# Performance work log

Hardware: AMD Instinct MI355X
Metric: run time of the kernel (lower is better)

The kernel has to match this reference:

```python
import jax, jax.numpy as jnp
import numpy as np

NMS_RADIUS = 2.0   # cfgs.NMS_radius (meters)
EPS = 1e-6         # torch nn.PairwiseDistance default eps (added to the diff)
M = 16384          # number of keypoint candidates
SCENE = 100.0      # scene extent in meters


def setup_inputs() -> dict:
    key = jax.random.key(0)
    k1, k2 = jax.random.split(key)
    nodes = jax.random.uniform(k1, (M, 3), dtype=jnp.float32) * SCENE
    overlap_score = jax.random.normal(k2, (M,), dtype=jnp.float32)
    return {"nodes": nodes, "overlap_score": overlap_score}


def _greedy_nms(nodes, radius):
    """Sequential greedy NMS: keep node i iff its distance to every
    already-kept node exceeds radius. Faithful to the torch loop:
    (dis > radius).sum() == n_kept  <=>  all kept dists > radius."""
    n = nodes.shape[0]

    def body(i, mask):
        # torch nn.PairwiseDistance computes ||x1 - x2 + eps||_2
        d = jnp.linalg.norm(nodes[i] - nodes + EPS, axis=-1)  # [n]
        keep = jnp.all(jnp.where(mask, d > radius, True))
        return mask.at[i].set(keep)

    mask0 = jnp.zeros(n, dtype=bool).at[0].set(True)
    return jax.lax.fori_loop(1, n, body, mask0)


def reference(nodes, overlap_score):
    # sort by overlap score descending, run greedy NMS, unsort the mask
    order = jnp.argsort(-overlap_score)
    mask_sorted = _greedy_nms(nodes[order], NMS_RADIUS)
    mask = jnp.zeros_like(mask_sorted).at[order].set(mask_sorted)
    nms_length = mask.sum(dtype=jnp.int32)[None]
    return mask, nms_length
```

## Files before the change

### kernel.cpp

```cpp
#include <hip/hip_runtime.h>


#define M_PTS    16384
#define RADIUS   2.0f
#define EPS_D    1e-6f
#define GRID_N   25
#define NCELLS   (GRID_N * GRID_N * GRID_N)
#define CELL_CAP 12
#define K_NBR    12
#define CELLS_PB (GRID_N * GRID_N)
#define LIST_PB  (CELLS_PB * CELL_CAP)
#define EPT      5
#define ACT_PAD  (EPT * 1024)
#define SENT     M_PTS


__device__ __forceinline__ int cell_of(float v) {
  int c = (int)(v * 0.25f);
  return c < 0 ? 0 : (c > GRID_N - 1 ? GRID_N - 1 : c);
}

__device__ __forceinline__ bool edge_test(float4 pi, float4 pj, int j, int i) {
  bool earlier = (pj.w > pi.w) || ((pj.w == pi.w) && (j < i));
  if (!earlier) return false;
  float ddx = __fadd_rn(__fsub_rn(pi.x, pj.x), EPS_D);
  float ddy = __fadd_rn(__fsub_rn(pi.y, pj.y), EPS_D);
  float ddz = __fadd_rn(__fsub_rn(pi.z, pj.z), EPS_D);
  float d2 = __fadd_rn(__fadd_rn(__fmul_rn(ddx, ddx), __fmul_rn(ddy, ddy)),
                       __fmul_rn(ddz, ddz));
  return !(__fsqrt_rn(d2) > RADIUS);
}

__global__ __launch_bounds__(1024) void bin25(
    const float* __restrict__ nodes, const float* __restrict__ score,
    float4* __restrict__ pts, int* __restrict__ cell_cnt,
    unsigned short* __restrict__ cell_list) {
  __shared__ int ccnt[CELLS_PB];
  __shared__ unsigned short clist[LIST_PB];
  const int tid = threadIdx.x;
  const int b   = blockIdx.x;
  if (tid < CELLS_PB) ccnt[tid] = 0;
  __syncthreads();

  for (int i = tid; i < M_PTS; i += 1024) {
    float x = nodes[3 * i + 0];
    if (cell_of(x) != b) continue;
    float y = nodes[3 * i + 1];
    float z = nodes[3 * i + 2];
    float s = score[i];
    pts[i] = make_float4(x, y, z, s);
    int lc = cell_of(y) * GRID_N + cell_of(z);
    int pos = atomicAdd(&ccnt[lc], 1);
    if (pos < CELL_CAP) clist[lc * CELL_CAP + pos] = (unsigned short)i;
  }
  __syncthreads();

  if (tid < CELLS_PB) {
    int v = ccnt[tid];
    cell_cnt[b * CELLS_PB + tid] = v > CELL_CAP ? CELL_CAP : v;
  }
  for (int e = tid; e < LIST_PB; e += 1024)
    cell_list[b * LIST_PB + e] = clist[e];
}

__global__ __launch_bounds__(256) void wscan(
    const float4* __restrict__ pts, const int* __restrict__ cell_cnt,
    const unsigned short* __restrict__ cell_list,
    int* __restrict__ cnt, unsigned short* __restrict__ nbr,
    int* __restrict__ out) {
  const int tid  = threadIdx.x;
  const int lane = tid & 63;
  const int d    = lane & 31;
  const int half = lane >> 5;
  const int gwave = (blockIdx.x * 256 + tid) >> 6;
  const int i = gwave * 2 + half;

  const float4 pi = pts[i];
  int n = 0, cid = 0, m = 0, firstj = 0;
  if (d < 27) {
    int cx = cell_of(pi.x) + d / 9 - 1;
    int cy = cell_of(pi.y) + (d / 3) % 3 - 1;
    int cz = cell_of(pi.z) + d % 3 - 1;
    if (cx >= 0 && cx < GRID_N && cy >= 0 && cy < GRID_N &&
        cz >= 0 && cz < GRID_N) {
      cid = (cx * GRID_N + cy) * GRID_N + cz;
      m = cell_cnt[cid];
      for (int s = 0; s < m; ++s) {
        int j = cell_list[cid * CELL_CAP + s];
        if (edge_test(pi, pts[j], j, i)) { if (!n) firstj = j; ++n; }
      }
    }
  }
  int x = n;
#pragma unroll
  for (int off = 1; off < 32; off <<= 1) {
    int y = __shfl_up(x, off, 32);
    if (d >= off) x += y;
  }
  int excl = x - n;
  int tot = __shfl(x, 31, 32);
  if (n == 1) {
    if (excl < K_NBR) nbr[i * K_NBR + excl] = (unsigned short)firstj;
  } else if (n > 1) {
    int pos = excl;
    for (int s = 0; s < m && pos < K_NBR; ++s) {
      int j = cell_list[cid * CELL_CAP + s];
      if (edge_test(pi, pts[j], j, i)) {
        nbr[i * K_NBR + pos] = (unsigned short)j;
        ++pos;
      }
    }
  }
  if (d == 0) {
    cnt[i] = tot > K_NBR ? K_NBR : tot;
    if (tot == 0) out[i] = 1;
  }
}

__global__ __launch_bounds__(1024) void solve_nb(
    const int* __restrict__ cnt, const unsigned short* __restrict__ nbr,
    int* __restrict__ out, int out_size) {
  __shared__ unsigned char mask[M_PTS + 4];
  __shared__ unsigned int act[ACT_PAD];
  __shared__ int act_n, total;

  const int tid = threadIdx.x;
  const int lane = tid & 63;
  if (tid == 0) { act_n = 0; total = 0; }
  unsigned int* mask4 = (unsigned int*)mask;
  for (int w = tid; w < M_PTS / 4; w += 1024) mask4[w] = 0x01010101u;
  if (tid == 0) mask4[M_PTS / 4] = 0u;
  for (int a = tid; a < ACT_PAD; a += 1024) act[a] = 0u;
  __syncthreads();

  for (int k = tid; k < M_PTS; k += 1024) {
    int c = cnt[k];
    if (c > K_NBR) c = K_NBR;
    unsigned long long b = __ballot(c > 0);
    int wcnt = __popcll(b);
    int wbase = 0;
    if (lane == 0 && wcnt) wbase = atomicAdd(&act_n, wcnt);
    wbase = __shfl(wbase, 0, 64);
    if (c > 0) {
      int pos = wbase + __popcll(b & ((1ull << lane) - 1ull));
      if (pos < ACT_PAD) act[pos] = (unsigned)k | ((unsigned)c << 16);
    }
  }
  __syncthreads();
  const int na = act_n;
  const bool ok = (na <= ACT_PAD);

  unsigned ae[EPT];
  unsigned short r0[EPT], r1[EPT], r2[EPT];
  int cur[EPT];
#pragma unroll
  for (int e = 0; e < EPT; ++e) {
    unsigned v = act[tid + e * 1024];
    ae[e] = v;
    int k = (int)(v & 0xFFFFu);
    int c = (int)(v >> 16);
    const unsigned short* row = nbr + (size_t)k * K_NBR;
    unsigned w = (c > 0) ? *(const unsigned int*)row : 0u;
    r0[e] = (c > 0) ? (unsigned short)(w & 0xFFFFu) : (unsigned short)SENT;
    r1[e] = (c > 1) ? (unsigned short)(w >> 16)     : (unsigned short)SENT;
    r2[e] = (c > 2) ? row[2]                        : (unsigned short)SENT;
    cur[e] = 1;
  }
  __syncthreads();

  if (ok) {
    for (int it = 0; it < 96; ++it) {
      int m0[EPT], m1[EPT], m2[EPT];
#pragma unroll
      for (int e = 0; e < EPT; ++e) m0[e] = (int)mask[r0[e]];
#pragma unroll
      for (int e = 0; e < EPT; ++e) m1[e] = (int)mask[r1[e]];
#pragma unroll
      for (int e = 0; e < EPT; ++e) m2[e] = (int)mask[r2[e]];
      int any = 0;
#pragma unroll
      for (int e = 0; e < EPT; ++e) {
        unsigned v = ae[e];
        int c = (int)(v >> 16);
        if (!c) continue;
        int kp = (m0[e] ^ 1) & (m1[e] ^ 1) & (m2[e] ^ 1);
        if (c > 3) {
          int k = (int)(v & 0xFFFFu);
          const unsigned short* row = nbr + (size_t)k * K_NBR;
          for (int t = 3; t < c; ++t) kp &= (int)mask[row[t]] ^ 1;
        }
        if (kp != cur[e]) {
          cur[e] = kp;
          mask[v & 0xFFFFu] = (unsigned char)kp;
          any = 1;
        }
      }
      if (__syncthreads_count(any) == 0) break;
    }
    int ks = 0;
#pragma unroll
    for (int e = 0; e < EPT; ++e) {
      unsigned v = ae[e];
      if ((v >> 16) != 0u) {
        out[v & 0xFFFFu] = cur[e];
        ks += cur[e];
      }
    }
#pragma unroll
    for (int off = 32; off > 0; off >>= 1) ks += __shfl_down(ks, off, 64);
    if (lane == 0) atomicAdd(&total, ks);
    __syncthreads();
    if (tid == 0) out[out_size - 1] = (M_PTS - na) + total;
  } else {
    __shared__ int changed;
    for (int it = 0; it < 512; ++it) {
      if (tid == 0) changed = 0;
      __syncthreads();
      int any = 0;
      for (int k = tid; k < M_PTS; k += 1024) {
        int c = cnt[k]; if (c > K_NBR) c = K_NBR;
        if (!c) continue;
        int kp = 1;
        for (int t = 0; t < c; ++t) kp &= (int)mask[nbr[k * K_NBR + t]] ^ 1;
        if (kp != (int)mask[k]) { mask[k] = (unsigned char)kp; any = 1; }
      }
      if (any) changed = 1;
      __syncthreads();
      if (!changed) break;
    }
    __syncthreads();
    int ks = 0;
    for (int k = tid; k < M_PTS; k += 1024) {
      int m = (int)mask[k];
      out[k] = m;
      ks += m;
    }
#pragma unroll
    for (int off = 32; off > 0; off >>= 1) ks += __shfl_down(ks, off, 64);
    if (lane == 0) atomicAdd(&total, ks);
    __syncthreads();
    if (tid == 0) out[out_size - 1] = total;
  }
}

extern "C" void kernel_launch(void* const* d_in, const int* in_sizes, int n_in,
                              void* d_out, int out_size, void* d_ws, size_t ws_size,
                              hipStream_t stream) {
  const float* nodes = (const float*)d_in[0];
  const float* score = (const float*)d_in[1];
  int* out = (int*)d_out;

  char* ws = (char*)d_ws;
  float4* pts = (float4*)ws;
  int* cell_cnt = (int*)(ws + 262144);
  int* cnt = (int*)(ws + 327680);
  unsigned short* cell_list = (unsigned short*)(ws + 393216);
  unsigned short* nbr = (unsigned short*)(ws + 770048);

  bin25<<<GRID_N, 1024, 0, stream>>>(nodes, score, pts, cell_cnt, cell_list);
  wscan<<<2048, 256, 0, stream>>>(pts, cell_cnt, cell_list, cnt, nbr, out);
  solve_nb<<<1, 1024, 0, stream>>>(cnt, nbr, out, out_size);
}
```

Baseline: 39.43 us.

## Split active NMS nodes by degree and double-pump relaxation per barrier

The single-block fixed-point solver now sorts active nodes into two compact lists: nodes with exactly one earlier neighbour, stored as 16-bit ids with a cached neighbour, and nodes with two or more neighbours. Each iteration runs two relaxation sweeps between block-wide barriers, with a lower iteration cap. This aims to cut the number of __syncthreads_count barriers and to make the common single-neighbour case cheaper in registers and shared-memory reads. The cost is more work per barrier, and there is a risk of overflow into the slow fallback if either list exceeds its capacity.

```diff
diff --git a/kernel.cpp b/kernel.cpp
--- a/kernel.cpp
+++ b/kernel.cpp
@@ -10,9 +10,12 @@
 #define K_NBR    12
 #define CELLS_PB (GRID_N * GRID_N)
 #define LIST_PB  (CELLS_PB * CELL_CAP)
-#define EPT      5
-#define ACT_PAD  (EPT * 1024)
+#define EPT1     4
+#define C1_PAD   (EPT1 * 1024)
+#define EPT2     2
+#define C2_PAD   (EPT2 * 1024)
 #define SENT     M_PTS
+#define NOK1     0xFFFFu
 
 
 __device__ __forceinline__ int cell_of(float v) {
@@ -117,45 +120,69 @@
   }
 }
 
-__global__ __launch_bounds__(1024) void solve_nb(
+__global__ __launch_bounds__(1024) void solve_sp(
     const int* __restrict__ cnt, const unsigned short* __restrict__ nbr,
     int* __restrict__ out, int out_size) {
   __shared__ unsigned char mask[M_PTS + 4];
-  __shared__ unsigned int act[ACT_PAD];
-  __shared__ int act_n, total;
+  __shared__ unsigned short act1[C1_PAD];
+  __shared__ unsigned int  act2[C2_PAD];
+  __shared__ int n1_, n2_, total;
 
   const int tid = threadIdx.x;
   const int lane = tid & 63;
-  if (tid == 0) { act_n = 0; total = 0; }
+  if (tid == 0) { n1_ = 0; n2_ = 0; total = 0; }
   unsigned int* mask4 = (unsigned int*)mask;
   for (int w = tid; w < M_PTS / 4; w += 1024) mask4[w] = 0x01010101u;
   if (tid == 0) mask4[M_PTS / 4] = 0u;
-  for (int a = tid; a < ACT_PAD; a += 1024) act[a] = 0u;
+  unsigned int* act1w = (unsigned int*)act1;
+  for (int a = tid; a < C1_PAD / 2; a += 1024) act1w[a] = 0xFFFFFFFFu;
+  for (int a = tid; a < C2_PAD; a += 1024) act2[a] = 0u;
   __syncthreads();
 
   for (int k = tid; k < M_PTS; k += 1024) {
     int c = cnt[k];
     if (c > K_NBR) c = K_NBR;
-    unsigned long long b = __ballot(c > 0);
-    int wcnt = __popcll(b);
-    int wbase = 0;
-    if (lane == 0 && wcnt) wbase = atomicAdd(&act_n, wcnt);
-    wbase = __shfl(wbase, 0, 64);
-    if (c > 0) {
-      int pos = wbase + __popcll(b & ((1ull << lane) - 1ull));
-      if (pos < ACT_PAD) act[pos] = (unsigned)k | ((unsigned)c << 16);
-    }
-  }
-  __syncthreads();
-  const int na = act_n;
-  const bool ok = (na <= ACT_PAD);
-
-  unsigned ae[EPT];
-  unsigned short r0[EPT], r1[EPT], r2[EPT];
-  int cur[EPT];
-#pragma unroll
-  for (int e = 0; e < EPT; ++e) {
-    unsigned v = act[tid + e * 1024];
+    bool s1 = (c == 1), s2 = (c >= 2);
+    unsigned long long b1 = __ballot(s1);
+    if (b1) {
+      int wbase = 0;
+      if (lane == 0) wbase = atomicAdd(&n1_, __popcll(b1));
+      wbase = __shfl(wbase, 0, 64);
+      if (s1) {
+        int pos = wbase + __popcll(b1 & ((1ull << lane) - 1ull));
+        if (pos < C1_PAD) act1[pos] = (unsigned short)k;
+      }
+    }
+    unsigned long long b2 = __ballot(s2);
+    if (b2) {
+      int wbase = 0;
+      if (lane == 0) wbase = atomicAdd(&n2_, __popcll(b2));
+      wbase = __shfl(wbase, 0, 64);
+      if (s2) {
+        int pos = wbase + __popcll(b2 & ((1ull << lane) - 1ull));
+        if (pos < C2_PAD) act2[pos] = (unsigned)k | ((unsigned)c << 16);
+      }
+    }
+  }
+  __syncthreads();
+  const int n1 = n1_, n2 = n2_;
+  const bool ok = (n1 <= C1_PAD) && (n2 <= C2_PAD);
+
+  unsigned short k1[EPT1], q0[EPT1];
+  int cur1[EPT1];
+#pragma unroll
+  for (int e = 0; e < EPT1; ++e) {
+    unsigned short k = act1[tid + e * 1024];
+    k1[e] = k;
+    q0[e] = (k != NOK1) ? nbr[(size_t)k * K_NBR] : (unsigned short)SENT;
+    cur1[e] = 1;
+  }
+  unsigned ae[EPT2];
+  unsigned short r0[EPT2], r1[EPT2], r2[EPT2];
+  int cur2[EPT2];
+#pragma unroll
+  for (int e = 0; e < EPT2; ++e) {
+    unsigned v = act2[tid + e * 1024];
     ae[e] = v;
     int k = (int)(v & 0xFFFFu);
     int c = (int)(v >> 16);
@@ -164,53 +191,75 @@
     r0[e] = (c > 0) ? (unsigned short)(w & 0xFFFFu) : (unsigned short)SENT;
     r1[e] = (c > 1) ? (unsigned short)(w >> 16)     : (unsigned short)SENT;
     r2[e] = (c > 2) ? row[2]                        : (unsigned short)SENT;
-    cur[e] = 1;
+    cur2[e] = 1;
   }
   __syncthreads();
 
   if (ok) {
-    for (int it = 0; it < 96; ++it) {
-      int m0[EPT], m1[EPT], m2[EPT];
-#pragma unroll
-      for (int e = 0; e < EPT; ++e) m0[e] = (int)mask[r0[e]];
-#pragma unroll
-      for (int e = 0; e < EPT; ++e) m1[e] = (int)mask[r1[e]];
-#pragma unroll
-      for (int e = 0; e < EPT; ++e) m2[e] = (int)mask[r2[e]];
+    for (int it = 0; it < 48; ++it) {
       int any = 0;
 #pragma unroll
-      for (int e = 0; e < EPT; ++e) {
-        unsigned v = ae[e];
-        int c = (int)(v >> 16);
-        if (!c) continue;
-        int kp = (m0[e] ^ 1) & (m1[e] ^ 1) & (m2[e] ^ 1);
-        if (c > 3) {
-          int k = (int)(v & 0xFFFFu);
-          const unsigned short* row = nbr + (size_t)k * K_NBR;
-          for (int t = 3; t < c; ++t) kp &= (int)mask[row[t]] ^ 1;
+      for (int pump = 0; pump < 2; ++pump) {
+        int p0[EPT1];
+#pragma unroll
+        for (int e = 0; e < EPT1; ++e) p0[e] = (int)mask[q0[e]];
+        int m0[EPT2], m1[EPT2], m2[EPT2];
+#pragma unroll
+        for (int e = 0; e < EPT2; ++e) m0[e] = (int)mask[r0[e]];
+#pragma unroll
+        for (int e = 0; e < EPT2; ++e) m1[e] = (int)mask[r1[e]];
+#pragma unroll
+        for (int e = 0; e < EPT2; ++e) m2[e] = (int)mask[r2[e]];
+#pragma unroll
+        for (int e = 0; e < EPT1; ++e) {
+          int kp = p0[e] ^ 1;
+          if (kp != cur1[e]) {
+            cur1[e] = kp;
+            mask[k1[e]] = (unsigned char)kp;
+            any = 1;
+          }
         }
-        if (kp != cur[e]) {
-          cur[e] = kp;
-          mask[v & 0xFFFFu] = (unsigned char)kp;
-          any = 1;
+#pragma unroll
+        for (int e = 0; e < EPT2; ++e) {
+          unsigned v = ae[e];
+          int c = (int)(v >> 16);
+          if (!c) continue;
+          int kp = (m0[e] ^ 1) & (m1[e] ^ 1) & (m2[e] ^ 1);
+          if (c > 3) {
+            int k = (int)(v & 0xFFFFu);
+            const unsigned short* row = nbr + (size_t)k * K_NBR;
+            for (int t = 3; t < c; ++t) kp &= (int)mask[row[t]] ^ 1;
+          }
+          if (kp != cur2[e]) {
+            cur2[e] = kp;
+            mask[v & 0xFFFFu] = (unsigned char)kp;
+            any = 1;
+          }
         }
       }
       if (__syncthreads_count(any) == 0) break;
     }
     int ks = 0;
 #pragma unroll
-    for (int e = 0; e < EPT; ++e) {
+    for (int e = 0; e < EPT1; ++e) {
+      if (k1[e] != NOK1) {
+        out[k1[e]] = cur1[e];
+        ks += cur1[e];
+      }
+    }
+#pragma unroll
+    for (int e = 0; e < EPT2; ++e) {
       unsigned v = ae[e];
       if ((v >> 16) != 0u) {
-        out[v & 0xFFFFu] = cur[e];
-        ks += cur[e];
+        out[v & 0xFFFFu] = cur2[e];
+        ks += cur2[e];
       }
     }
 #pragma unroll
     for (int off = 32; off > 0; off >>= 1) ks += __shfl_down(ks, off, 64);
     if (lane == 0) atomicAdd(&total, ks);
     __syncthreads();
-    if (tid == 0) out[out_size - 1] = (M_PTS - na) + total;
+    if (tid == 0) out[out_size - 1] = (M_PTS - (n1 + n2)) + total;
   } else {
     __shared__ int changed;
     for (int it = 0; it < 512; ++it) {
@@ -259,5 +308,5 @@
 
   bin25<<<GRID_N, 1024, 0, stream>>>(nodes, score, pts, cell_cnt, cell_list);
   wscan<<<2048, 256, 0, stream>>>(pts, cell_cnt, cell_list, cnt, nbr, out);
-  solve_nb<<<1, 1024, 0, stream>>>(cnt, nbr, out, out_size);
-}
+  solve_sp<<<1, 1024, 0, stream>>>(cnt, nbr, out, out_size);
+}
```

Measured after the change: 42.22 us. 7.1% more time.
